# Kernel optimization log

Measured on AMD Instinct MI355X. Metric: run time of the kernel, lower is better.

The kernel has to match this reference:

```python
import jax, jax.numpy as jnp
import numpy as np

B, S, H, W, DF, D, HID, ITERS = 8, 8, 64, 64, 64, 64, 128, 3
EPS = 1e-8


def build_grid(h, w):
    ranges = [np.linspace(-1.0, 1.0, num=h), np.linspace(-1.0, 1.0, num=w)]
    g = np.meshgrid(*ranges, sparse=False, indexing='xy')
    return jnp.asarray(np.stack(g, axis=-1), dtype=jnp.float32)  # [H, W, 2]


def ln(x, g, b):
    m = jnp.mean(x, axis=-1, keepdims=True)
    v = jnp.mean((x - m) ** 2, axis=-1, keepdims=True)
    return (x - m) * jax.lax.rsqrt(v + 1e-5) * g + b


def setup_inputs() -> dict:
    key = jax.random.key(0)
    ks = iter(jax.random.split(key, 64))
    def nrm(shape, s=0.02):
        return jax.random.normal(next(ks), shape, jnp.float32) * s
    inp = {}
    inp['inputs'] = jax.random.normal(next(ks), (B, H, W, DF), jnp.float32)
    # learned slot inits and learned per-slot position / scale factors
    inp['slots_p'] = jax.random.normal(next(ks), (1, S, D), jnp.float32)
    inp['s_pos_p'] = 2.0 * jax.random.uniform(next(ks), (1, S, 2), jnp.float32) - 1.0
    inp['s_scale_p'] = 0.1 + 0.01 * jax.random.normal(next(ks), (1, S, 2), jnp.float32)
    # soft position embedding Linear(2, D)
    inp['W_pos'] = nrm((2, D)); inp['b_pos'] = jnp.zeros((D,), jnp.float32)
    # q/k/v projections
    inp['Wq'] = nrm((D, D)); inp['bq'] = jnp.zeros((D,), jnp.float32)
    inp['Wk'] = nrm((DF, D)); inp['bk'] = jnp.zeros((D,), jnp.float32)
    inp['Wv'] = nrm((DF, D)); inp['bv'] = jnp.zeros((D,), jnp.float32)
    # layernorms
    inp['g_in'] = jnp.ones((DF,), jnp.float32); inp['b_in'] = jnp.zeros((DF,), jnp.float32)
    inp['g_slots'] = jnp.ones((D,), jnp.float32); inp['b_slots'] = jnp.zeros((D,), jnp.float32)
    inp['g_k'] = jnp.ones((D,), jnp.float32); inp['b_k'] = jnp.zeros((D,), jnp.float32)
    inp['g_v'] = jnp.ones((D,), jnp.float32); inp['b_v'] = jnp.zeros((D,), jnp.float32)
    # shared kv MLP fc1_kv / fc2_kv
    inp['W1'] = nrm((D, 2 * D)); inp['b1'] = jnp.zeros((2 * D,), jnp.float32)
    inp['W2'] = nrm((2 * D, D)); inp['b2'] = jnp.zeros((D,), jnp.float32)
    # GRUCell (torch layout transposed to [in, 3*D])
    inp['W_ih'] = nrm((D, 3 * D)); inp['b_ih'] = jnp.zeros((3 * D,), jnp.float32)
    inp['W_hh'] = nrm((D, 3 * D)); inp['b_hh'] = jnp.zeros((3 * D,), jnp.float32)
    # residual slot MLP
    inp['g_pre'] = jnp.ones((D,), jnp.float32); inp['b_pre'] = jnp.zeros((D,), jnp.float32)
    inp['Wf1'] = nrm((D, HID)); inp['bf1'] = jnp.zeros((HID,), jnp.float32)
    inp['Wf2'] = nrm((HID, D)); inp['bf2'] = jnp.zeros((D,), jnp.float32)
    return inp


def reference(inputs, slots_p, s_pos_p, s_scale_p, W_pos, b_pos, Wq, bq, Wk, bk, Wv, bv,
              g_in, b_in, g_slots, b_slots, g_k, b_k, g_v, b_v, W1, b1, W2, b2,
              W_ih, W_hh, b_ih, b_hh, g_pre, b_pre, Wf1, bf1, Wf2, bf2):
    grid = build_grid(H, W)                 # [H, W, 2]
    grid_flat = grid.reshape(-1, 2)          # [HW, 2]
    scale = D ** (-0.5)

    x = ln(inputs, g_in, b_in)
    k0 = x @ Wk + bk                         # [B, H, W, D]
    v0 = x @ Wv + bv

    slots = jnp.broadcast_to(slots_p, (B, S, D))
    s_pos = jnp.clip(jnp.broadcast_to(s_pos_p, (B, S, 2)), -1.0, 1.0)[:, :, None, None, :]
    s_scale = jnp.clip(jnp.broadcast_to(s_scale_p, (B, S, 2)), 1e-3, 2.0)[:, :, None, None, :]

    def proj_kv(base, sp, ss, g, b):
        gr = (grid[None, None] - sp) / (ss * 5.0)      # [B, S, H, W, 2]
        pe = gr @ W_pos + b_pos                        # [B, S, H, W, D]
        t = (base[:, None] + pe).reshape(B, S, H * W, D)
        t = ln(t, g, b)
        return jax.nn.relu(t @ W1 + b1) @ W2 + b2      # [B, S, HW, D]

    for i in range(ITERS + 1):
        slots_prev = slots
        q = ln(slots, g_slots, b_slots) @ Wq + bq       # [B, S, D]
        kk = proj_kv(k0, s_pos, s_scale, g_k, b_k)
        vv = proj_kv(v0, s_pos, s_scale, g_v, b_v)
        dots = jnp.einsum('bid,bijd->bij', q, kk) * scale
        attn_mask = jax.nn.softmax(dots, axis=1) + EPS  # softmax over slot axis
        attn = attn_mask / jnp.sum(attn_mask, axis=-1, keepdims=True)
        updates = jnp.einsum('bijd,bij->bid', vv, attn)
        if i < ITERS:
            xg = updates.reshape(-1, D) @ W_ih + b_ih
            hg = slots_prev.reshape(-1, D) @ W_hh + b_hh
            ir, iz, inn = jnp.split(xg, 3, axis=-1)
            hr, hz, hn = jnp.split(hg, 3, axis=-1)
            r = jax.nn.sigmoid(ir + hr)
            z = jax.nn.sigmoid(iz + hz)
            n = jnp.tanh(inn + r * hn)
            slots = ((1.0 - z) * n + z * slots_prev.reshape(-1, D)).reshape(B, S, D)
            slots = slots + (jax.nn.relu(ln(slots, g_pre, b_pre) @ Wf1 + bf1) @ Wf2 + bf2)
        else:
            slots = slots_prev
        # update per-slot position / scale from the attention mask
        sp = jnp.einsum('bij,jd->bid', attn_mask, grid_flat) / jnp.sum(attn_mask, axis=-1, keepdims=True)
        diff = grid_flat[None, None] - sp[:, :, None]   # [B, S, HW, 2]
        am = attn_mask + 1e-8
        ss = jnp.sqrt(jnp.einsum('bij,bijd->bid', am, diff ** 2) / jnp.sum(am, axis=-1, keepdims=True))
        s_pos = sp[:, :, None, None, :]
        s_scale = jnp.clip(ss, 1e-3, 2.0)[:, :, None, None, :]
    return slots, s_pos, s_scale, attn_mask
```

## Files before the change

kernel.cpp:

```cpp
#include <hip/hip_runtime.h>
#include <math.h>

typedef __bf16 bf16_t;
typedef __bf16 bfrag __attribute__((ext_vector_type(8)));
typedef float ffrag __attribute__((ext_vector_type(4)));

__device__ __forceinline__ float wave_sum(float v) {
#pragma unroll
  for (int m = 32; m >= 1; m >>= 1) v += __shfl_xor(v, m, 64);
  return v;
}
__device__ __forceinline__ float lin_(int i) { return -1.f + (2.f * (float)i) / 63.f; }
__device__ __forceinline__ float bflo(unsigned u) { return __uint_as_float(u << 16); }
__device__ __forceinline__ float bfhi(unsigned u) { return __uint_as_float(u & 0xFFFF0000u); }

__device__ __forceinline__ void pass_type(
    const bf16_t xs[][72], bf16_t t0s[][72],
    const bf16_t WTl[][72], const bf16_t W1l[][72],
    const float* __restrict__ bias, const float* wpxs, const float* wpys,
    const float* bpvs, float* __restrict__ statsG, bf16_t* __restrict__ P0G,
    int j0, int wv, int lq, int ln15) {
  ffrag C[4] = {{0,0,0,0},{0,0,0,0},{0,0,0,0},{0,0,0,0}};
#pragma unroll
  for (int ks = 0; ks < 2; ++ks) {
    bfrag a = *(const bfrag*)&xs[wv * 16 + ln15][ks * 32 + lq * 8];
#pragma unroll
    for (int nt = 0; nt < 4; ++nt) {
      bfrag bb = *(const bfrag*)&WTl[nt * 16 + ln15][ks * 32 + lq * 8];
      C[nt] = __builtin_amdgcn_mfma_f32_16x16x32_bf16(a, bb, C[nt], 0, 0, 0);
    }
  }
  float kv[4][4];
  float st[5][4];
#pragma unroll
  for (int i = 0; i < 5; ++i)
#pragma unroll
    for (int rg = 0; rg < 4; ++rg) st[i][rg] = 0.f;
#pragma unroll
  for (int nt = 0; nt < 4; ++nt) {
    int n = nt * 16 + ln15;
    float bn = bias[n], pxw = wpxs[n], pyw = wpys[n], bpw = bpvs[n];
#pragma unroll
    for (int rg = 0; rg < 4; ++rg) {
      float v = C[nt][rg] + bn;
      kv[nt][rg] = v;
      st[0][rg] += v; st[1][rg] += v * v; st[2][rg] += v * pxw;
      st[3][rg] += v * pyw; st[4][rg] += v * bpw;
    }
  }
#pragma unroll
  for (int i = 0; i < 5; ++i)
#pragma unroll
    for (int rg = 0; rg < 4; ++rg) {
      float v = st[i][rg];
      v += __shfl_xor(v, 1, 64); v += __shfl_xor(v, 2, 64);
      v += __shfl_xor(v, 4, 64); v += __shfl_xor(v, 8, 64);
      st[i][rg] = v;
    }
  if (ln15 == 0) {
#pragma unroll
    for (int rg = 0; rg < 4; ++rg) {
      int j = j0 + wv * 16 + lq * 4 + rg;
#pragma unroll
      for (int i = 0; i < 5; ++i) statsG[j * 5 + i] = st[i][rg];
    }
  }
#pragma unroll
  for (int nt = 0; nt < 4; ++nt)
#pragma unroll
    for (int rg = 0; rg < 4; ++rg)
      t0s[wv * 16 + lq * 4 + rg][nt * 16 + ln15] = (bf16_t)kv[nt][rg];
  ffrag D[8] = {{0,0,0,0},{0,0,0,0},{0,0,0,0},{0,0,0,0},
                {0,0,0,0},{0,0,0,0},{0,0,0,0},{0,0,0,0}};
#pragma unroll
  for (int ks = 0; ks < 2; ++ks) {
    bfrag a = *(const bfrag*)&t0s[wv * 16 + ln15][ks * 32 + lq * 8];
#pragma unroll
    for (int nt = 0; nt < 8; ++nt) {
      bfrag bb = *(const bfrag*)&W1l[nt * 16 + ln15][ks * 32 + lq * 8];
      D[nt] = __builtin_amdgcn_mfma_f32_16x16x32_bf16(a, bb, D[nt], 0, 0, 0);
    }
  }
#pragma unroll
  for (int nt = 0; nt < 8; ++nt)
#pragma unroll
    for (int rg = 0; rg < 4; ++rg)
      P0G[(size_t)(j0 + wv * 16 + lq * 4 + rg) * 128 + nt * 16 + ln15] =
          (bf16_t)D[nt][rg];
}

__global__ __launch_bounds__(256) void k_pre(
    const float* __restrict__ inp, const float* __restrict__ g_in,
    const float* __restrict__ b_in, const float* __restrict__ bk,
    const float* __restrict__ bv, const float* __restrict__ Wk,
    const float* __restrict__ Wv, const float* __restrict__ W1,
    const float* __restrict__ b1, const float* __restrict__ g_k,
    const float* __restrict__ b_k, const float* __restrict__ g_v,
    const float* __restrict__ b_v, const float* __restrict__ W_pos,
    const float* __restrict__ b_pos, const float* __restrict__ slots_p,
    const float* __restrict__ s_pos_p, const float* __restrict__ s_scale_p,
    const float* __restrict__ g_slots, const float* __restrict__ b_slots,
    const float* __restrict__ Wq, const float* __restrict__ bq,
    const float* __restrict__ W2, const float* __restrict__ b2,
    bf16_t* __restrict__ P0k, bf16_t* __restrict__ P0v,
    float* __restrict__ statsK, float* __restrict__ statsV,
    float* __restrict__ w2qg, float* __restrict__ b2qg,
    float* __restrict__ slotsS, float* __restrict__ sposS,
    float* __restrict__ sscaleS, float* __restrict__ momentsHsum,
    float4* __restrict__ nckA, float* __restrict__ nckB,
    float4* __restrict__ ncvA, float* __restrict__ ncvB,
    float* __restrict__ possum, unsigned* __restrict__ ctr) {
  __shared__ bf16_t xs[64][72];
  __shared__ bf16_t t0s[64][72];
  __shared__ bf16_t WkTl[64][72];
  __shared__ bf16_t WvTl[64][72];
  __shared__ bf16_t W1kl[128][72];
  __shared__ bf16_t W1vl[128][72];
  __shared__ float wpxs[64], wpys[64], bpvs[64];
  const int tid = threadIdx.x;
  const int j0 = blockIdx.x * 64;
  for (int i = tid; i < 4096; i += 256) {
    int n = i >> 6, d = i & 63;
    WkTl[n][d] = (bf16_t)Wk[d * 64 + n];
    WvTl[n][d] = (bf16_t)Wv[d * 64 + n];
  }
  for (int i = tid; i < 8192; i += 256) {
    int n = i >> 6, c = i & 63;
    float w = W1[c * 128 + n];
    W1kl[n][c] = (bf16_t)(g_k[c] * w);
    W1vl[n][c] = (bf16_t)(g_v[c] * w);
  }
  if (tid < 64) { wpxs[tid] = W_pos[tid]; wpys[tid] = W_pos[64 + tid]; bpvs[tid] = b_pos[tid]; }
  {
    const int px = tid >> 2, cg = tid & 3;
    const float* rowp = inp + (size_t)(j0 + px) * 64 + cg * 16;
    float v[16];
    *(float4*)&v[0]  = ((const float4*)rowp)[0];
    *(float4*)&v[4]  = ((const float4*)rowp)[1];
    *(float4*)&v[8]  = ((const float4*)rowp)[2];
    *(float4*)&v[12] = ((const float4*)rowp)[3];
    float s = 0.f, s2 = 0.f;
#pragma unroll
    for (int i = 0; i < 16; ++i) { s += v[i]; s2 += v[i] * v[i]; }
    s += __shfl_xor(s, 1, 64); s += __shfl_xor(s, 2, 64);
    s2 += __shfl_xor(s2, 1, 64); s2 += __shfl_xor(s2, 2, 64);
    float m = s * 0.015625f;
    float r = rsqrtf(s2 * 0.015625f - m * m + 1e-5f);
    float g[16], bb[16];
    *(float4*)&g[0]  = ((const float4*)(g_in + cg * 16))[0];
    *(float4*)&g[4]  = ((const float4*)(g_in + cg * 16))[1];
    *(float4*)&g[8]  = ((const float4*)(g_in + cg * 16))[2];
    *(float4*)&g[12] = ((const float4*)(g_in + cg * 16))[3];
    *(float4*)&bb[0]  = ((const float4*)(b_in + cg * 16))[0];
    *(float4*)&bb[4]  = ((const float4*)(b_in + cg * 16))[1];
    *(float4*)&bb[8]  = ((const float4*)(b_in + cg * 16))[2];
    *(float4*)&bb[12] = ((const float4*)(b_in + cg * 16))[3];
#pragma unroll
    for (int e = 0; e < 8; ++e) {
      float x0 = (v[2 * e] - m) * r * g[2 * e] + bb[2 * e];
      float x1 = (v[2 * e + 1] - m) * r * g[2 * e + 1] + bb[2 * e + 1];
      union { unsigned u; bf16_t h[2]; } cv;
      cv.h[0] = (bf16_t)x0; cv.h[1] = (bf16_t)x1;
      *(unsigned*)&xs[px][cg * 16 + 2 * e] = cv.u;
    }
  }
  __syncthreads();
  const int wv = tid >> 6, lane = tid & 63, lq = lane >> 4, ln15 = lane & 15;
  pass_type(xs, t0s, WkTl, W1kl, bk, wpxs, wpys, bpvs, statsK, P0k, j0, wv, lq, ln15);
  pass_type(xs, t0s, WvTl, W1vl, bv, wpxs, wpys, bpvs, statsV, P0v, j0, wv, lq, ln15);
  if (blockIdx.x < 64 && tid < 64) {
    int bs = blockIdx.x, d = tid;
    float v = slots_p[(bs & 7) * 64 + d];
    float m = wave_sum(v) * 0.015625f;
    float c = v - m;
    float var = wave_sum(c * c) * 0.015625f;
    float xn = c * rsqrtf(var + 1e-5f) * g_slots[d] + b_slots[d];
    float q = bq[d];
    for (int cc = 0; cc < 64; ++cc) q = fmaf(__shfl(xn, cc, 64), Wq[cc * 64 + d], q);
    float w0 = 0.f, w1 = 0.f;
    for (int cc = 0; cc < 64; ++cc) {
      float qc = __shfl(q, cc, 64);
      w0 = fmaf(W2[d * 64 + cc], qc, w0);
      w1 = fmaf(W2[(64 + d) * 64 + cc], qc, w1);
    }
    w2qg[bs * 128 + d] = w0;
    w2qg[bs * 128 + 64 + d] = w1;
    float p = wave_sum(b2[d] * q);
    if (d == 0) b2qg[bs] = p;
  }
  if (blockIdx.x == 0) {
    for (int i = tid; i < 8512; i += 256) momentsHsum[i] = 0.f;
    if (tid < 8) ctr[tid] = 0u;
    for (int i = tid; i < 4096; i += 256) slotsS[i] = slots_p[i & 511];
    if (tid < 128) {
      sposS[tid] = fminf(fmaxf(s_pos_p[tid & 15], -1.f), 1.f);
      sscaleS[tid] = fminf(fmaxf(s_scale_p[tid & 15], 0.001f), 2.f);
    }
    if (tid < 128) {
      int n = tid;
      float wxk = 0, wyk = 0, wbk = 0, uk = 0, sk = 0;
      float wxv = 0, wyv = 0, wbv = 0, uv = 0, sv = 0;
      for (int c = 0; c < 64; ++c) {
        float w = W1[c * 128 + n];
        float wk = g_k[c] * w, wvv = g_v[c] * w;
        float px = W_pos[c], py = W_pos[64 + c], bp = b_pos[c];
        wxk += px * wk; wyk += py * wk; wbk += bp * wk; sk += wk; uk += b_k[c] * w;
        wxv += px * wvv; wyv += py * wvv; wbv += bp * wvv; sv += wvv; uv += b_v[c] * w;
      }
      nckA[n] = make_float4(wxk, wyk, wbk, uk + b1[n]); nckB[n] = sk;
      ncvA[n] = make_float4(wxv, wyv, wbv, uv + b1[n]); ncvB[n] = sv;
    }
    if (tid < 64) {
      float px = W_pos[tid], py = W_pos[64 + tid], bp = b_pos[tid];
      float sarr[9] = {px, py, bp, px * px, py * py, bp * bp, px * py, px * bp, py * bp};
#pragma unroll
      for (int i = 0; i < 9; ++i) {
        float v2 = wave_sum(sarr[i]);
        if (tid == 0) possum[i] = v2;
      }
    }
  }
}

template <int LAST>
__global__ __launch_bounds__(256) void k_iter(
    const bf16_t* __restrict__ P0kg, const bf16_t* __restrict__ P0vg,
    const float* __restrict__ statsK, const float* __restrict__ statsV,
    const float4* __restrict__ nckA, const float* __restrict__ nckB,
    const float4* __restrict__ ncvA, const float* __restrict__ ncvB,
    const float* __restrict__ possum, const float* __restrict__ w2qg,
    const float* __restrict__ b2qg, const float* __restrict__ sposS,
    const float* __restrict__ sscaleS, float* __restrict__ moments,
    float* __restrict__ Hsum, float* __restrict__ outAttn,
    const float* __restrict__ slotsS, float* __restrict__ outSlots,
    float* __restrict__ outSpos, float* __restrict__ outSscale,
    unsigned* __restrict__ ctr) {
  __shared__ unsigned Pbuf[64 * 65];
  __shared__ float nck12[64][12];
  __shared__ float w2q16[64][16];
  __shared__ float4 scalV[64][9];
  __shared__ float attnS[64][10];
  __shared__ float HsumT[8][128];
  __shared__ float momAcc[8][5];
  __shared__ unsigned s_done;
  const int tid = threadIdx.x;
  const int tile = blockIdx.x, b = blockIdx.y;
  const int jg0 = b * 4096 + tile * 64;
#pragma unroll
  for (int r = 0; r < 4; ++r) {
    int idx = tid + 256 * r;
    int row = idx >> 4, seg = idx & 15;
    uint4 v = ((const uint4*)P0kg)[(size_t)(jg0 + row) * 16 + seg];
    unsigned* dst = &Pbuf[row * 65 + seg * 4];
    dst[0] = v.x; dst[1] = v.y; dst[2] = v.z; dst[3] = v.w;
  }
  if (tid < 128) {
    int n = tid, k = n >> 1, h = n & 1;
    int kp = ((k & 15) << 2) | (k >> 4);
    float4 A = nckA[n];
    *(float4*)&nck12[kp][h * 4] = A;
    nck12[kp][8 + h] = nckB[n];
  }
#pragma unroll
  for (int r = 0; r < 4; ++r) {
    int idx = tid + 256 * r;
    int s = idx >> 7, n = idx & 127;
    int k = n >> 1, h = n & 1;
    int kp = ((k & 15) << 2) | (k >> 4);
    w2q16[kp][h * 8 + s] = w2qg[(b * 8 + s) * 128 + n];
  }
  if (!LAST) {
#pragma unroll
    for (int r = 0; r < 4; ++r) ((float*)HsumT)[tid + 256 * r] = 0.f;
  }
  if (tid < 40) momAcc[tid / 5][tid % 5] = 0.f;
  float4 ncv0 = {0, 0, 0, 0}, ncv1 = {0, 0, 0, 0};
  float wsv0 = 0.f, wsv1 = 0.f;
  if (!LAST) {
    int l = tid & 63;
    ncv0 = ncvA[l]; ncv1 = ncvA[l + 64];
    wsv0 = ncvB[l]; wsv1 = ncvB[l + 64];
  }
  __syncthreads();

  const int px = tid >> 2, sp = tid & 3;
  const int jimg = tile * 64 + px;
  const float gx = lin_(jimg & 63), gy = lin_(jimg >> 6);
  const float Swx = possum[0], Swy = possum[1], Sbp = possum[2];
  const float Swx2 = possum[3], Swy2 = possum[4], Sbp2 = possum[5];
  const float Swxy = possum[6], Swxb = possum[7], Swyb = possum[8];
  float skA[5], svA[5];
#pragma unroll
  for (int i = 0; i < 5; ++i) {
    skA[i] = statsK[(size_t)(jg0 + px) * 5 + i];
    if (!LAST) svA[i] = statsV[(size_t)(jg0 + px) * 5 + i];
  }
  float c1a[8], c2a[8], rKa[8], mrKa[8];
#pragma unroll
  for (int s = 0; s < 8; ++s) {
    int bs = b * 8 + s;
    float spx = sposS[bs * 2], spy = sposS[bs * 2 + 1];
    float rxx = 1.f / (sscaleS[bs * 2] * 5.f);
    float ryy = 1.f / (sscaleS[bs * 2 + 1] * 5.f);
    float c1 = (gx - spx) * rxx, c2 = (gy - spy) * ryy;
    float quad = c1 * c1 * Swx2 + c2 * c2 * Swy2 + Sbp2 +
                 2.f * (c1 * c2 * Swxy + c1 * Swxb + c2 * Swyb);
    float mK = (skA[0] + c1 * Swx + c2 * Swy + Sbp) * 0.015625f;
    float e2K = (skA[1] + 2.f * (c1 * skA[2] + c2 * skA[3] + skA[4]) + quad) * 0.015625f;
    float rK = rsqrtf(e2K - mK * mK + 1e-5f);
    c1a[s] = c1; c2a[s] = c2; rKa[s] = rK; mrKa[s] = mK * rK;
    if (!LAST && (s >> 1) == sp) {
      float mV = (svA[0] + c1 * Swx + c2 * Swy + Sbp) * 0.015625f;
      float e2V = (svA[1] + 2.f * (c1 * svA[2] + c2 * svA[3] + svA[4]) + quad) * 0.015625f;
      float rV = rsqrtf(e2V - mV * mV + 1e-5f);
      scalV[px][s] = make_float4(c1, c2, rV, mV * rV);
    }
  }
  float d8[8] = {0, 0, 0, 0, 0, 0, 0, 0};
#pragma unroll 4
  for (int i = 0; i < 16; ++i) {
    int k = sp * 16 + i;
    unsigned u = Pbuf[px * 65 + k];
    float p0 = bflo(u), p1 = bfhi(u);
    const int kp = (i << 2) | sp;
    const float* nr = &nck12[kp][0];
    float4 A0 = *(const float4*)nr;
    float4 A1 = *(const float4*)(nr + 4);
    float ws0 = nr[8], ws1 = nr[9];
    const float* wr = &w2q16[kp][0];
    float4 q0a = *(const float4*)wr;
    float4 q0b = *(const float4*)(wr + 4);
    float4 q1a = *(const float4*)(wr + 8);
    float4 q1b = *(const float4*)(wr + 12);
    float qq0[8] = {q0a.x, q0a.y, q0a.z, q0a.w, q0b.x, q0b.y, q0b.z, q0b.w};
    float qq1[8] = {q1a.x, q1a.y, q1a.z, q1a.w, q1b.x, q1b.y, q1b.z, q1b.w};
    float bm0 = p0 + A0.z, bm1 = p1 + A1.z;
#pragma unroll
    for (int s = 0; s < 8; ++s) {
      float z0 = bm0 + c1a[s] * A0.x + c2a[s] * A0.y;
      float h0 = fmaxf(fmaf(rKa[s], z0, fmaf(-mrKa[s], ws0, A0.w)), 0.f);
      d8[s] = fmaf(h0, qq0[s], d8[s]);
      float z1 = bm1 + c1a[s] * A1.x + c2a[s] * A1.y;
      float h1 = fmaxf(fmaf(rKa[s], z1, fmaf(-mrKa[s], ws1, A1.w)), 0.f);
      d8[s] = fmaf(h1, qq1[s], d8[s]);
    }
  }
#pragma unroll
  for (int s = 0; s < 8; ++s) {
    float v = d8[s];
    v += __shfl_xor(v, 1, 64);
    v += __shfl_xor(v, 2, 64);
    d8[s] = (v + b2qg[b * 8 + s]) * 0.125f;
  }
  float mx = d8[0];
#pragma unroll
  for (int s = 1; s < 8; ++s) mx = fmaxf(mx, d8[s]);
  float tt = 0.f;
  float e8[8];
#pragma unroll
  for (int s = 0; s < 8; ++s) { e8[s] = expf(d8[s] - mx); tt += e8[s]; }
  float inv = 1.f / tt;
#pragma unroll
  for (int s = 0; s < 8; ++s) e8[s] = e8[s] * inv + 1e-8f;
  float wa, wb;
  if (sp == 0) { wa = e8[0]; wb = e8[1]; }
  else if (sp == 1) { wa = e8[2]; wb = e8[3]; }
  else if (sp == 2) { wa = e8[4]; wb = e8[5]; }
  else { wa = e8[6]; wb = e8[7]; }
  *(float2*)&attnS[px][sp * 2] = make_float2(wa, wb);
  if (LAST) {
    outAttn[(size_t)(b * 8 + sp * 2) * 4096 + jimg] = wa;
    outAttn[(size_t)(b * 8 + sp * 2 + 1) * 4096 + jimg] = wb;
  }
  {
    float mm[10] = {wa, wa * gx, wa * gy, wa * gx * gx, wa * gy * gy,
                    wb, wb * gx, wb * gy, wb * gx * gx, wb * gy * gy};
#pragma unroll
    for (int i = 0; i < 10; ++i) {
      float v = mm[i];
      v += __shfl_xor(v, 4, 64); v += __shfl_xor(v, 8, 64);
      v += __shfl_xor(v, 16, 64); v += __shfl_xor(v, 32, 64);
      mm[i] = v;
    }
    if ((tid & 63) < 4) {
#pragma unroll
      for (int i = 0; i < 5; ++i) {
        atomicAdd(&momAcc[sp * 2][i], mm[i]);
        atomicAdd(&momAcc[sp * 2 + 1][i], mm[5 + i]);
      }
    }
  }
  __syncthreads();

  if (!LAST) {
#pragma unroll
    for (int r = 0; r < 4; ++r) {
      int idx = tid + 256 * r;
      int row = idx >> 4, seg = idx & 15;
      uint4 v = ((const uint4*)P0vg)[(size_t)(jg0 + row) * 16 + seg];
      unsigned* dst = &Pbuf[row * 65 + seg * 4];
      dst[0] = v.x; dst[1] = v.y; dst[2] = v.z; dst[3] = v.w;
    }
    __syncthreads();
    const int w = tid >> 6, l = tid & 63;
    float hacc[8][2];
#pragma unroll
    for (int s = 0; s < 8; ++s) { hacc[s][0] = 0.f; hacc[s][1] = 0.f; }
    const unsigned short* P16 = (const unsigned short*)Pbuf;
#pragma unroll 2
    for (int i = 0; i < 16; ++i) {
      int j = w * 16 + i;
      float pv0 = __uint_as_float((unsigned)P16[j * 130 + l] << 16);
      float pv1 = __uint_as_float((unsigned)P16[j * 130 + 64 + l] << 16);
      float bm0 = pv0 + ncv0.z, bm1 = pv1 + ncv1.z;
#pragma unroll
      for (int s = 0; s < 8; ++s) {
        float4 sc = scalV[j][s];
        float aw = attnS[j][s];
        float z0 = bm0 + sc.x * ncv0.x + sc.y * ncv0.y;
        float h0 = fmaxf(fmaf(sc.z, z0, fmaf(-sc.w, wsv0, ncv0.w)), 0.f);
        hacc[s][0] = fmaf(aw, h0, hacc[s][0]);
        float z1 = bm1 + sc.x * ncv1.x + sc.y * ncv1.y;
        float h1 = fmaxf(fmaf(sc.z, z1, fmaf(-sc.w, wsv1, ncv1.w)), 0.f);
        hacc[s][1] = fmaf(aw, h1, hacc[s][1]);
      }
    }
#pragma unroll
    for (int s = 0; s < 8; ++s) {
      atomicAdd(&HsumT[s][l], hacc[s][0]);
      atomicAdd(&HsumT[s][l + 64], hacc[s][1]);
    }
    __syncthreads();
#pragma unroll
    for (int r = 0; r < 4; ++r) {
      int i2 = tid + 256 * r;
      int s = i2 >> 7, n = i2 & 127;
      atomicAdd(&Hsum[(b * 8 + s) * 128 + n], HsumT[s][n]);
    }
  }
  if (tid < 40)
    atomicAdd(&moments[(b * 8 + tid / 5) * 5 + tid % 5], momAcc[tid / 5][tid % 5]);

  if (LAST) {
    __syncthreads();
    __threadfence();
    if (tid == 0) s_done = atomicAdd(&ctr[b], 1u);
    __syncthreads();
    if (s_done != 63) return;
    __threadfence();
    if (tid < 40)
      momAcc[tid / 5][tid % 5] = atomicAdd(&moments[(b * 8 + tid / 5) * 5 + tid % 5], 0.f);
    __syncthreads();
    if (tid < 8) {
      int s = tid, bs = b * 8 + s;
      float M0 = momAcc[s][0], M1x = momAcc[s][1], M1y = momAcc[s][2];
      float M2x = momAcc[s][3], M2y = momAcc[s][4];
      float invM0 = 1.f / M0;
      float spx2 = M1x * invM0, spy2 = M1y * invM0;
      float M0a = M0 + 4096.f * 1e-8f;
      float G2 = 1408.6772487f * 1e-8f;
      float vx = (M2x + G2 - 2.f * spx2 * M1x + spx2 * spx2 * M0a) / M0a;
      float vy = (M2y + G2 - 2.f * spy2 * M1y + spy2 * spy2 * M0a) / M0a;
      float ssx = fminf(fmaxf(sqrtf(fmaxf(vx, 0.f)), 0.001f), 2.f);
      float ssy = fminf(fmaxf(sqrtf(fmaxf(vy, 0.f)), 0.001f), 2.f);
      outSpos[bs * 2] = spx2; outSpos[bs * 2 + 1] = spy2;
      outSscale[bs * 2] = ssx; outSscale[bs * 2 + 1] = ssy;
    }
    for (int i = tid; i < 512; i += 256)
      outSlots[b * 512 + i] = slotsS[b * 512 + i];
  }
}

__global__ __launch_bounds__(192) void k_fin(
    float* __restrict__ moments, float* __restrict__ Hsum,
    const float* __restrict__ W2, const float* __restrict__ b2,
    const float* __restrict__ W_ih, const float* __restrict__ b_ih,
    const float* __restrict__ W_hh, const float* __restrict__ b_hh,
    const float* __restrict__ g_pre, const float* __restrict__ b_pre,
    const float* __restrict__ Wf1, const float* __restrict__ bf1,
    const float* __restrict__ Wf2, const float* __restrict__ bf2,
    const float* __restrict__ g_slots, const float* __restrict__ b_slots,
    const float* __restrict__ Wq, const float* __restrict__ bq,
    float* __restrict__ slotsS, float* __restrict__ sposS, float* __restrict__ sscaleS,
    float* __restrict__ w2qg, float* __restrict__ b2qg) {
  const int bs = blockIdx.x;
  const int t = threadIdx.x;
  __shared__ float hsum_s[128], upd[64], sprev[64], xg[192], hg[192];
  __shared__ float snew[64], xpre[64], hf[128], sfin[64], xn[64], qsh[64];
  const float M0 = moments[bs * 5 + 0];
  const float M1x = moments[bs * 5 + 1], M1y = moments[bs * 5 + 2];
  const float M2x = moments[bs * 5 + 3], M2y = moments[bs * 5 + 4];
  const float invM0 = 1.f / M0;
  const float spx = M1x * invM0, spy = M1y * invM0;
  const float M0a = M0 + 4096.f * 1e-8f;
  const float G2 = 1408.6772487f * 1e-8f;
  const float vx = (M2x + G2 - 2.f * spx * M1x + spx * spx * M0a) / M0a;
  const float vy = (M2y + G2 - 2.f * spy * M1y + spy * spy * M0a) / M0a;
  float ssx = fminf(fmaxf(sqrtf(fmaxf(vx, 0.f)), 0.001f), 2.f);
  float ssy = fminf(fmaxf(sqrtf(fmaxf(vy, 0.f)), 0.001f), 2.f);
  if (t == 0) {
    sposS[bs * 2 + 0] = spx; sposS[bs * 2 + 1] = spy;
    sscaleS[bs * 2 + 0] = ssx; sscaleS[bs * 2 + 1] = ssy;
  }
  if (t < 128) hsum_s[t] = Hsum[bs * 128 + t];
  if (t < 64) sprev[t] = slotsS[bs * 64 + t];
  __syncthreads();
  if (t < 128) Hsum[bs * 128 + t] = 0.f;
  if (t < 5) moments[bs * 5 + t] = 0.f;
  if (t < 64) {
    float a = 0.f;
#pragma unroll
    for (int k = 0; k < 128; ++k) a += hsum_s[k] * W2[k * 64 + t];
    upd[t] = a * invM0 + b2[t];
  }
  __syncthreads();
  {
    float a = b_ih[t], h = b_hh[t];
#pragma unroll
    for (int d = 0; d < 64; ++d) {
      a += upd[d] * W_ih[d * 192 + t];
      h += sprev[d] * W_hh[d * 192 + t];
    }
    xg[t] = a; hg[t] = h;
  }
  __syncthreads();
  if (t < 64) {
    float r = 1.f / (1.f + expf(-(xg[t] + hg[t])));
    float z = 1.f / (1.f + expf(-(xg[64 + t] + hg[64 + t])));
    float n = tanhf(xg[128 + t] + r * hg[128 + t]);
    snew[t] = (1.f - z) * n + z * sprev[t];
  }
  __syncthreads();
  if (t < 64) {
    float v = snew[t];
    float m = wave_sum(v) * 0.015625f;
    float c = v - m;
    float var = wave_sum(c * c) * 0.015625f;
    xpre[t] = c * rsqrtf(var + 1e-5f) * g_pre[t] + b_pre[t];
  }
  __syncthreads();
  if (t < 128) {
    float a = bf1[t];
#pragma unroll
    for (int d = 0; d < 64; ++d) a += xpre[d] * Wf1[d * 128 + t];
    hf[t] = fmaxf(a, 0.f);
  }
  __syncthreads();
  if (t < 64) {
    float a = bf2[t];
#pragma unroll
    for (int k = 0; k < 128; ++k) a += hf[k] * Wf2[k * 64 + t];
    float nv = snew[t] + a;
    slotsS[bs * 64 + t] = nv;
    sfin[t] = nv;
  }
  __syncthreads();
  if (t < 64) {
    float v = sfin[t];
    float m = wave_sum(v) * 0.015625f;
    float c = v - m;
    float var = wave_sum(c * c) * 0.015625f;
    xn[t] = c * rsqrtf(var + 1e-5f) * g_slots[t] + b_slots[t];
  }
  __syncthreads();
  if (t < 64) {
    float a = bq[t];
#pragma unroll
    for (int d = 0; d < 64; ++d) a += xn[d] * Wq[d * 64 + t];
    qsh[t] = a;
  }
  __syncthreads();
  if (t < 128) {
    float a = 0.f;
#pragma unroll
    for (int d = 0; d < 64; ++d) a += W2[t * 64 + d] * qsh[d];
    w2qg[bs * 128 + t] = a;
  }
  if (t < 64) {
    float p = wave_sum(b2[t] * qsh[t]);
    if (t == 0) b2qg[bs] = p;
  }
}

extern "C" void kernel_launch(void* const* d_in, const int* in_sizes, int n_in,
                              void* d_out, int out_size, void* d_ws, size_t ws_size,
                              hipStream_t stream) {
  const float* const* in = (const float* const*)d_in;
  float* ws = (float*)d_ws;
  bf16_t* P0k   = (bf16_t*)(ws + 0);
  bf16_t* P0v   = (bf16_t*)(ws + 2097152);
  float* statsK = ws + 4194304;
  float* statsV = ws + 4358144;
  float* w2qg   = ws + 4521984;
  float* b2qg   = ws + 4530176;
  float* slotsS = ws + 4530240;
  float* sposS  = ws + 4534336;
  float* sscaleS= ws + 4534464;
  float* moments= ws + 4534592;
  float* Hsum   = ws + 4534912;
  float4* nckA  = (float4*)(ws + 4543104);
  float* nckB   = ws + 4543616;
  float4* ncvA  = (float4*)(ws + 4543744);
  float* ncvB   = ws + 4544256;
  float* possum = ws + 4544384;
  unsigned* ctr = (unsigned*)(ws + 4544400);

  float* out = (float*)d_out;
  float* outSlots  = out;
  float* outSpos   = out + 4096;
  float* outSscale = out + 4224;
  float* outAttn   = out + 4352;

  k_pre<<<512, 256, 0, stream>>>(
      in[0], in[12], in[13], in[9], in[11], in[8], in[10], in[20], in[21],
      in[16], in[17], in[18], in[19], in[4], in[5], in[1], in[2], in[3],
      in[14], in[15], in[6], in[7], in[22], in[23],
      P0k, P0v, statsK, statsV, w2qg, b2qg,
      slotsS, sposS, sscaleS, moments, nckA, nckB, ncvA, ncvB, possum, ctr);
  for (int i = 0; i < 3; ++i) {
    k_iter<0><<<dim3(64, 8), 256, 0, stream>>>(
        P0k, P0v, statsK, statsV, nckA, nckB, ncvA, ncvB, possum,
        w2qg, b2qg, sposS, sscaleS, moments, Hsum, outAttn,
        slotsS, outSlots, outSpos, outSscale, ctr);
    k_fin<<<64, 192, 0, stream>>>(moments, Hsum, in[22], in[23], in[24], in[25],
                                  in[26], in[27], in[28], in[29], in[30], in[31],
                                  in[32], in[33], in[14], in[15], in[6], in[7],
                                  slotsS, sposS, sscaleS, w2qg, b2qg);
  }
  k_iter<1><<<dim3(64, 8), 256, 0, stream>>>(
      P0k, P0v, statsK, statsV, nckA, nckB, ncvA, ncvB, possum,
      w2qg, b2qg, sposS, sscaleS, moments, Hsum, outAttn,
      slotsS, outSlots, outSpos, outSscale, ctr);
}
```

Measured before the change: 333.1 us.

## Halve k_iter tile size, replicate atomic accumulators, prefetch V tile early

k_iter now handles 32 pixels per block instead of 64, doubling the grid to 128x8, and each thread owns one slot instead of two. Global Hsum and moment atomics are spread over 8 replica buffers (picked by tile index) to cut atomic contention, and k_fin and the last block sum the replicas. The V tile is loaded into registers before the attention phase to hide its latency. Zeroing of the larger replica buffers moves to all k_pre blocks. The cost is more blocks, duplicated per-block setup, and extra reduction reads in k_fin.

```diff
diff --git a/kernel.cpp b/kernel.cpp
--- a/kernel.cpp
+++ b/kernel.cpp
@@ -106,7 +106,7 @@
     float* __restrict__ statsK, float* __restrict__ statsV,
     float* __restrict__ w2qg, float* __restrict__ b2qg,
     float* __restrict__ slotsS, float* __restrict__ sposS,
-    float* __restrict__ sscaleS, float* __restrict__ momentsHsum,
+    float* __restrict__ sscaleS, float* __restrict__ HsumRmomR,
     float4* __restrict__ nckA, float* __restrict__ nckB,
     float4* __restrict__ ncvA, float* __restrict__ ncvB,
     float* __restrict__ possum, unsigned* __restrict__ ctr) {
@@ -119,6 +119,10 @@
   __shared__ float wpxs[64], wpys[64], bpvs[64];
   const int tid = threadIdx.x;
   const int j0 = blockIdx.x * 64;
+  {
+    int i = blockIdx.x * 256 + tid;
+    if (i < 69632) HsumRmomR[i] = 0.f;
+  }
   for (int i = tid; i < 4096; i += 256) {
     int n = i >> 6, d = i & 63;
     WkTl[n][d] = (bf16_t)Wk[d * 64 + n];
@@ -189,7 +193,6 @@
     if (d == 0) b2qg[bs] = p;
   }
   if (blockIdx.x == 0) {
-    for (int i = tid; i < 8512; i += 256) momentsHsum[i] = 0.f;
     if (tid < 8) ctr[tid] = 0u;
     for (int i = tid; i < 4096; i += 256) slotsS[i] = slots_p[i & 511];
     if (tid < 128) {
@@ -230,50 +233,57 @@
     const float4* __restrict__ ncvA, const float* __restrict__ ncvB,
     const float* __restrict__ possum, const float* __restrict__ w2qg,
     const float* __restrict__ b2qg, const float* __restrict__ sposS,
-    const float* __restrict__ sscaleS, float* __restrict__ moments,
-    float* __restrict__ Hsum, float* __restrict__ outAttn,
+    const float* __restrict__ sscaleS, float* __restrict__ HsumR,
+    float* __restrict__ momR, float* __restrict__ outAttn,
     const float* __restrict__ slotsS, float* __restrict__ outSlots,
     float* __restrict__ outSpos, float* __restrict__ outSscale,
     unsigned* __restrict__ ctr) {
-  __shared__ unsigned Pbuf[64 * 65];
+  __shared__ unsigned Pbuf[32 * 65];
   __shared__ float nck12[64][12];
   __shared__ float w2q16[64][16];
-  __shared__ float4 scalV[64][9];
-  __shared__ float attnS[64][10];
+  __shared__ float4 scalV[32][9];
+  __shared__ float attnS[32][9];
   __shared__ float HsumT[8][128];
   __shared__ float momAcc[8][5];
+  __shared__ float bq_s[8];
   __shared__ unsigned s_done;
   const int tid = threadIdx.x;
   const int tile = blockIdx.x, b = blockIdx.y;
-  const int jg0 = b * 4096 + tile * 64;
-#pragma unroll
-  for (int r = 0; r < 4; ++r) {
+  const int rep = tile & 7;
+  const int jg0 = b * 4096 + tile * 32;
+#pragma unroll
+  for (int r = 0; r < 2; ++r) {
     int idx = tid + 256 * r;
     int row = idx >> 4, seg = idx & 15;
     uint4 v = ((const uint4*)P0kg)[(size_t)(jg0 + row) * 16 + seg];
     unsigned* dst = &Pbuf[row * 65 + seg * 4];
     dst[0] = v.x; dst[1] = v.y; dst[2] = v.z; dst[3] = v.w;
   }
+  uint4 vp0, vp1;
+  if (!LAST) {
+    vp0 = ((const uint4*)P0vg)[(size_t)(jg0 + (tid >> 4)) * 16 + (tid & 15)];
+    vp1 = ((const uint4*)P0vg)[(size_t)(jg0 + ((tid + 256) >> 4)) * 16 + ((tid + 256) & 15)];
+  }
   if (tid < 128) {
     int n = tid, k = n >> 1, h = n & 1;
-    int kp = ((k & 15) << 2) | (k >> 4);
-    float4 A = nckA[n];
-    *(float4*)&nck12[kp][h * 4] = A;
-    nck12[kp][8 + h] = nckB[n];
+    int rr = ((k & 7) << 3) | (k >> 3);
+    *(float4*)&nck12[rr][h * 4] = nckA[n];
+    nck12[rr][8 + h] = nckB[n];
   }
 #pragma unroll
   for (int r = 0; r < 4; ++r) {
     int idx = tid + 256 * r;
     int s = idx >> 7, n = idx & 127;
     int k = n >> 1, h = n & 1;
-    int kp = ((k & 15) << 2) | (k >> 4);
-    w2q16[kp][h * 8 + s] = w2qg[(b * 8 + s) * 128 + n];
+    int rr = ((k & 7) << 3) | (k >> 3);
+    w2q16[rr][h * 8 + s] = w2qg[(b * 8 + s) * 128 + n];
   }
   if (!LAST) {
 #pragma unroll
     for (int r = 0; r < 4; ++r) ((float*)HsumT)[tid + 256 * r] = 0.f;
   }
   if (tid < 40) momAcc[tid / 5][tid % 5] = 0.f;
+  if (tid < 8) bq_s[tid] = b2qg[b * 8 + tid];
   float4 ncv0 = {0, 0, 0, 0}, ncv1 = {0, 0, 0, 0};
   float wsv0 = 0.f, wsv1 = 0.f;
   if (!LAST) {
@@ -283,8 +293,8 @@
   }
   __syncthreads();
 
-  const int px = tid >> 2, sp = tid & 3;
-  const int jimg = tile * 64 + px;
+  const int px = tid >> 3, sp = tid & 7;
+  const int jimg = tile * 32 + px;
   const float gx = lin_(jimg & 63), gy = lin_(jimg >> 6);
   const float Swx = possum[0], Swy = possum[1], Sbp = possum[2];
   const float Swx2 = possum[3], Swy2 = possum[4], Sbp2 = possum[5];
@@ -309,25 +319,25 @@
     float e2K = (skA[1] + 2.f * (c1 * skA[2] + c2 * skA[3] + skA[4]) + quad) * 0.015625f;
     float rK = rsqrtf(e2K - mK * mK + 1e-5f);
     c1a[s] = c1; c2a[s] = c2; rKa[s] = rK; mrKa[s] = mK * rK;
-    if (!LAST && (s >> 1) == sp) {
+    if (!LAST && s == sp) {
       float mV = (svA[0] + c1 * Swx + c2 * Swy + Sbp) * 0.015625f;
       float e2V = (svA[1] + 2.f * (c1 * svA[2] + c2 * svA[3] + svA[4]) + quad) * 0.015625f;
       float rV = rsqrtf(e2V - mV * mV + 1e-5f);
-      scalV[px][s] = make_float4(c1, c2, rV, mV * rV);
+      scalV[px][sp] = make_float4(c1, c2, rV, mV * rV);
     }
   }
   float d8[8] = {0, 0, 0, 0, 0, 0, 0, 0};
 #pragma unroll 4
-  for (int i = 0; i < 16; ++i) {
-    int k = sp * 16 + i;
+  for (int i = 0; i < 8; ++i) {
+    int k = sp * 8 + i;
+    int rr = (i << 3) | sp;
     unsigned u = Pbuf[px * 65 + k];
     float p0 = bflo(u), p1 = bfhi(u);
-    const int kp = (i << 2) | sp;
-    const float* nr = &nck12[kp][0];
+    const float* nr = &nck12[rr][0];
     float4 A0 = *(const float4*)nr;
     float4 A1 = *(const float4*)(nr + 4);
     float ws0 = nr[8], ws1 = nr[9];
-    const float* wr = &w2q16[kp][0];
+    const float* wr = &w2q16[rr][0];
     float4 q0a = *(const float4*)wr;
     float4 q0b = *(const float4*)(wr + 4);
     float4 q1a = *(const float4*)(wr + 8);
@@ -350,7 +360,8 @@
     float v = d8[s];
     v += __shfl_xor(v, 1, 64);
     v += __shfl_xor(v, 2, 64);
-    d8[s] = (v + b2qg[b * 8 + s]) * 0.125f;
+    v += __shfl_xor(v, 4, 64);
+    d8[s] = (v + bq_s[s]) * 0.125f;
   }
   float mx = d8[0];
 #pragma unroll
@@ -359,47 +370,33 @@
   float e8[8];
 #pragma unroll
   for (int s = 0; s < 8; ++s) { e8[s] = expf(d8[s] - mx); tt += e8[s]; }
-  float inv = 1.f / tt;
-#pragma unroll
-  for (int s = 0; s < 8; ++s) e8[s] = e8[s] * inv + 1e-8f;
-  float wa, wb;
-  if (sp == 0) { wa = e8[0]; wb = e8[1]; }
-  else if (sp == 1) { wa = e8[2]; wb = e8[3]; }
-  else if (sp == 2) { wa = e8[4]; wb = e8[5]; }
-  else { wa = e8[6]; wb = e8[7]; }
-  *(float2*)&attnS[px][sp * 2] = make_float2(wa, wb);
-  if (LAST) {
-    outAttn[(size_t)(b * 8 + sp * 2) * 4096 + jimg] = wa;
-    outAttn[(size_t)(b * 8 + sp * 2 + 1) * 4096 + jimg] = wb;
-  }
+  float w0 = e8[sp] / tt + 1e-8f;
+  attnS[px][sp] = w0;
+  if (LAST) outAttn[(size_t)(b * 8 + sp) * 4096 + jimg] = w0;
   {
-    float mm[10] = {wa, wa * gx, wa * gy, wa * gx * gx, wa * gy * gy,
-                    wb, wb * gx, wb * gy, wb * gx * gx, wb * gy * gy};
-#pragma unroll
-    for (int i = 0; i < 10; ++i) {
+    float mm[5] = {w0, w0 * gx, w0 * gy, w0 * gx * gx, w0 * gy * gy};
+#pragma unroll
+    for (int i = 0; i < 5; ++i) {
       float v = mm[i];
-      v += __shfl_xor(v, 4, 64); v += __shfl_xor(v, 8, 64);
-      v += __shfl_xor(v, 16, 64); v += __shfl_xor(v, 32, 64);
+      v += __shfl_xor(v, 8, 64); v += __shfl_xor(v, 16, 64);
+      v += __shfl_xor(v, 32, 64);
       mm[i] = v;
     }
-    if ((tid & 63) < 4) {
-#pragma unroll
-      for (int i = 0; i < 5; ++i) {
-        atomicAdd(&momAcc[sp * 2][i], mm[i]);
-        atomicAdd(&momAcc[sp * 2 + 1][i], mm[5 + i]);
-      }
+    if ((tid & 63) < 8) {
+#pragma unroll
+      for (int i = 0; i < 5; ++i) atomicAdd(&momAcc[tid & 7][i], mm[i]);
     }
   }
   __syncthreads();
 
   if (!LAST) {
-#pragma unroll
-    for (int r = 0; r < 4; ++r) {
-      int idx = tid + 256 * r;
-      int row = idx >> 4, seg = idx & 15;
-      uint4 v = ((const uint4*)P0vg)[(size_t)(jg0 + row) * 16 + seg];
-      unsigned* dst = &Pbuf[row * 65 + seg * 4];
-      dst[0] = v.x; dst[1] = v.y; dst[2] = v.z; dst[3] = v.w;
+    {
+      int row0 = tid >> 4, seg0 = tid & 15;
+      unsigned* dst = &Pbuf[row0 * 65 + seg0 * 4];
+      dst[0] = vp0.x; dst[1] = vp0.y; dst[2] = vp0.z; dst[3] = vp0.w;
+      int row1 = (tid + 256) >> 4, seg1 = (tid + 256) & 15;
+      unsigned* d2 = &Pbuf[row1 * 65 + seg1 * 4];
+      d2[0] = vp1.x; d2[1] = vp1.y; d2[2] = vp1.z; d2[3] = vp1.w;
     }
     __syncthreads();
     const int w = tid >> 6, l = tid & 63;
@@ -408,8 +405,8 @@
     for (int s = 0; s < 8; ++s) { hacc[s][0] = 0.f; hacc[s][1] = 0.f; }
     const unsigned short* P16 = (const unsigned short*)Pbuf;
 #pragma unroll 2
-    for (int i = 0; i < 16; ++i) {
-      int j = w * 16 + i;
+    for (int i = 0; i < 8; ++i) {
+      int j = w * 8 + i;
       float pv0 = __uint_as_float((unsigned)P16[j * 130 + l] << 16);
       float pv1 = __uint_as_float((unsigned)P16[j * 130 + 64 + l] << 16);
       float bm0 = pv0 + ncv0.z, bm1 = pv1 + ncv1.z;
@@ -435,21 +432,27 @@
     for (int r = 0; r < 4; ++r) {
       int i2 = tid + 256 * r;
       int s = i2 >> 7, n = i2 & 127;
-      atomicAdd(&Hsum[(b * 8 + s) * 128 + n], HsumT[s][n]);
+      atomicAdd(&HsumR[(rep * 64 + b * 8 + s) * 128 + n], HsumT[s][n]);
     }
   }
   if (tid < 40)
-    atomicAdd(&moments[(b * 8 + tid / 5) * 5 + tid % 5], momAcc[tid / 5][tid % 5]);
+    atomicAdd(&momR[(rep * 64 + b * 8 + tid / 5) * 8 + tid % 5], momAcc[tid / 5][tid % 5]);
 
   if (LAST) {
     __syncthreads();
     __threadfence();
     if (tid == 0) s_done = atomicAdd(&ctr[b], 1u);
     __syncthreads();
-    if (s_done != 63) return;
+    if (s_done != 127) return;
     __threadfence();
-    if (tid < 40)
-      momAcc[tid / 5][tid % 5] = atomicAdd(&moments[(b * 8 + tid / 5) * 5 + tid % 5], 0.f);
+    if (tid < 40) {
+      int s = tid / 5, i = tid % 5;
+      float a = 0.f;
+#pragma unroll
+      for (int r = 0; r < 8; ++r)
+        a += atomicAdd(&momR[(r * 64 + b * 8 + s) * 8 + i], 0.f);
+      momAcc[s][i] = a;
+    }
     __syncthreads();
     if (tid < 8) {
       int s = tid, bs = b * 8 + s;
@@ -472,7 +475,7 @@
 }
 
 __global__ __launch_bounds__(192) void k_fin(
-    float* __restrict__ moments, float* __restrict__ Hsum,
+    float* __restrict__ HsumR, float* __restrict__ momR,
     const float* __restrict__ W2, const float* __restrict__ b2,
     const float* __restrict__ W_ih, const float* __restrict__ b_ih,
     const float* __restrict__ W_hh, const float* __restrict__ b_hh,
@@ -485,11 +488,34 @@
     float* __restrict__ w2qg, float* __restrict__ b2qg) {
   const int bs = blockIdx.x;
   const int t = threadIdx.x;
-  __shared__ float hsum_s[128], upd[64], sprev[64], xg[192], hg[192];
+  __shared__ float mom5[5], hsum_s[128], upd[64], sprev[64], xg[192], hg[192];
   __shared__ float snew[64], xpre[64], hf[128], sfin[64], xn[64], qsh[64];
-  const float M0 = moments[bs * 5 + 0];
-  const float M1x = moments[bs * 5 + 1], M1y = moments[bs * 5 + 2];
-  const float M2x = moments[bs * 5 + 3], M2y = moments[bs * 5 + 4];
+  if (t < 128) {
+    float a = 0.f;
+#pragma unroll
+    for (int r = 0; r < 8; ++r) a += HsumR[(r * 64 + bs) * 128 + t];
+    hsum_s[t] = a;
+  }
+  if (t >= 128 && t < 133) {
+    int i = t - 128;
+    float a = 0.f;
+#pragma unroll
+    for (int r = 0; r < 8; ++r) a += momR[(r * 64 + bs) * 8 + i];
+    mom5[i] = a;
+  }
+  if (t < 64) sprev[t] = slotsS[bs * 64 + t];
+  __syncthreads();
+  if (t < 128) {
+#pragma unroll
+    for (int r = 0; r < 8; ++r) HsumR[(r * 64 + bs) * 128 + t] = 0.f;
+  }
+  if (t >= 128 && t < 133) {
+    int i = t - 128;
+#pragma unroll
+    for (int r = 0; r < 8; ++r) momR[(r * 64 + bs) * 8 + i] = 0.f;
+  }
+  const float M0 = mom5[0], M1x = mom5[1], M1y = mom5[2];
+  const float M2x = mom5[3], M2y = mom5[4];
   const float invM0 = 1.f / M0;
   const float spx = M1x * invM0, spy = M1y * invM0;
   const float M0a = M0 + 4096.f * 1e-8f;
@@ -502,11 +528,6 @@
     sposS[bs * 2 + 0] = spx; sposS[bs * 2 + 1] = spy;
     sscaleS[bs * 2 + 0] = ssx; sscaleS[bs * 2 + 1] = ssy;
   }
-  if (t < 128) hsum_s[t] = Hsum[bs * 128 + t];
-  if (t < 64) sprev[t] = slotsS[bs * 64 + t];
-  __syncthreads();
-  if (t < 128) Hsum[bs * 128 + t] = 0.f;
-  if (t < 5) moments[bs * 5 + t] = 0.f;
   if (t < 64) {
     float a = 0.f;
 #pragma unroll
@@ -596,14 +617,14 @@
   float* slotsS = ws + 4530240;
   float* sposS  = ws + 4534336;
   float* sscaleS= ws + 4534464;
-  float* moments= ws + 4534592;
-  float* Hsum   = ws + 4534912;
-  float4* nckA  = (float4*)(ws + 4543104);
-  float* nckB   = ws + 4543616;
-  float4* ncvA  = (float4*)(ws + 4543744);
-  float* ncvB   = ws + 4544256;
-  float* possum = ws + 4544384;
-  unsigned* ctr = (unsigned*)(ws + 4544400);
+  float* HsumR  = ws + 4534592;
+  float* momR   = ws + 4600128;
+  float4* nckA  = (float4*)(ws + 4604224);
+  float* nckB   = ws + 4604736;
+  float4* ncvA  = (float4*)(ws + 4604864);
+  float* ncvB   = ws + 4605376;
+  float* possum = ws + 4605504;
+  unsigned* ctr = (unsigned*)(ws + 4605520);
 
   float* out = (float*)d_out;
   float* outSlots  = out;
@@ -616,19 +637,19 @@
       in[16], in[17], in[18], in[19], in[4], in[5], in[1], in[2], in[3],
       in[14], in[15], in[6], in[7], in[22], in[23],
       P0k, P0v, statsK, statsV, w2qg, b2qg,
-      slotsS, sposS, sscaleS, moments, nckA, nckB, ncvA, ncvB, possum, ctr);
+      slotsS, sposS, sscaleS, HsumR, nckA, nckB, ncvA, ncvB, possum, ctr);
   for (int i = 0; i < 3; ++i) {
-    k_iter<0><<<dim3(64, 8), 256, 0, stream>>>(
+    k_iter<0><<<dim3(128, 8), 256, 0, stream>>>(
         P0k, P0v, statsK, statsV, nckA, nckB, ncvA, ncvB, possum,
-        w2qg, b2qg, sposS, sscaleS, moments, Hsum, outAttn,
+        w2qg, b2qg, sposS, sscaleS, HsumR, momR, outAttn,
         slotsS, outSlots, outSpos, outSscale, ctr);
-    k_fin<<<64, 192, 0, stream>>>(moments, Hsum, in[22], in[23], in[24], in[25],
+    k_fin<<<64, 192, 0, stream>>>(HsumR, momR, in[22], in[23], in[24], in[25],
                                   in[26], in[27], in[28], in[29], in[30], in[31],
                                   in[32], in[33], in[14], in[15], in[6], in[7],
                                   slotsS, sposS, sscaleS, w2qg, b2qg);
   }
-  k_iter<1><<<dim3(64, 8), 256, 0, stream>>>(
+  k_iter<1><<<dim3(128, 8), 256, 0, stream>>>(
       P0k, P0v, statsK, statsV, nckA, nckB, ncvA, ncvB, possum,
-      w2qg, b2qg, sposS, sscaleS, moments, Hsum, outAttn,
+      w2qg, b2qg, sposS, sscaleS, HsumR, momR, outAttn,
       slotsS, outSlots, outSpos, outSscale, ctr);
 }
```

Result: slower. 403.7 us (+21.2%).
